# Kernel optimization log

Measured on AMD Instinct MI355X. Metric: run time of the kernel, lower is better.

Reference implementation:

```python
import jax, jax.numpy as jnp
import numpy as np

N, E, B, BLOCK = 100000, 1600000, 8, 12500
IN, HID, K, OUT = 128, 128, 4, 2
EPS = 1e-15


def setup_inputs() -> dict:
    key = jax.random.key(0)
    ks = jax.random.split(key, 14)
    x = jax.random.normal(ks[0], (N, IN), jnp.float32)
    # edges constrained within each graph's contiguous node block
    src = jax.random.randint(ks[1], (E,), 0, N)
    off = jax.random.randint(ks[2], (E,), 0, BLOCK)
    dst = (src // BLOCK) * BLOCK + off
    edge_index = jnp.stack([src, dst])
    batch = jnp.arange(N) // BLOCK
    s = 0.02
    params = dict(
        W_root1=jax.random.normal(ks[3], (IN, HID), jnp.float32) * s,
        W_rel1=jax.random.normal(ks[4], (IN, HID), jnp.float32) * s,
        b_rel1=jnp.zeros((HID,), jnp.float32),
        W_pool=jax.random.normal(ks[5], (HID, K), jnp.float32) * s,
        b_pool=jnp.zeros((K,), jnp.float32),
        W_rel3=jax.random.normal(ks[6], (HID, HID), jnp.float32) * s,
        b_rel3=jnp.zeros((HID,), jnp.float32),
        W_root3=jax.random.normal(ks[7], (HID, HID), jnp.float32) * s,
        W_lin1=jax.random.normal(ks[8], (HID, HID), jnp.float32) * s,
        b_lin1=jnp.zeros((HID,), jnp.float32),
        W_lin2=jax.random.normal(ks[9], (HID, OUT), jnp.float32) * s,
        b_lin2=jnp.zeros((OUT,), jnp.float32),
    )
    return dict(x=x, edge_index=edge_index, batch=batch, **params)


def _forward(x, edge_index, batch, W_root1, W_rel1, b_rel1, W_pool, b_pool,
             W_rel3, b_rel3, W_root3, W_lin1, b_lin1, W_lin2, b_lin2):
    src, dst = edge_index[0], edge_index[1]
    # GraphConv (aggr='add'): lin_rel(sum_j x_j) + lin_root(x)
    agg = jax.ops.segment_sum(x[src], dst, num_segments=N)  # [N, IN]
    h = jax.nn.relu(agg @ W_rel1 + b_rel1 + x @ W_root1)    # [N, HID]
    # cluster assignment
    s = jax.nn.softmax(h @ W_pool + b_pool, axis=-1)        # [N, K]
    # pooled node features: out[b] = S_b^T X_b  -> [B, K, HID]
    out = jax.ops.segment_sum(s[:, :, None] * h[:, None, :], batch, num_segments=B)
    # coarsened adjacency: out_adj[b] = S_b^T A_b S_b (A[dst, src] = 1 per edge)
    e_graph = batch[dst]
    contrib = s[dst][:, :, None] * s[src][:, None, :]       # [E, K, K]
    out_adj = jax.ops.segment_sum(contrib, e_graph, num_segments=B)  # [B, K, K]
    # mincut loss
    mincut_num = jnp.einsum('bkk->b', out_adj)
    deg = jax.ops.segment_sum(jnp.ones((E,), x.dtype), dst, num_segments=N)
    mincut_den = jax.ops.segment_sum(deg * jnp.sum(s * s, axis=-1), batch, num_segments=B)
    mc_loss = jnp.mean(-(mincut_num / mincut_den))
    # orthogonality loss
    ss = jax.ops.segment_sum(s[:, :, None] * s[:, None, :], batch, num_segments=B)  # [B,K,K]
    ss_norm = jnp.linalg.norm(ss, axis=(1, 2), keepdims=True)
    i_s = jnp.eye(K, dtype=x.dtype)
    o_loss = jnp.mean(jnp.linalg.norm(ss / ss_norm - i_s / jnp.sqrt(jnp.float32(K)), axis=(1, 2)))
    # fix and normalize coarsened adjacency
    out_adj = out_adj * (1.0 - i_s)  # zero diagonal
    d = jnp.sqrt(jnp.sum(out_adj, axis=-1)) + EPS  # [B, K]
    out_adj = out_adj / d[:, None, :] / d[:, :, None]
    # DenseGraphConv (aggr='add'): lin_rel(adj @ x) + lin_root(x)
    x2 = jnp.einsum('bkl,blc->bkc', out_adj, out) @ W_rel3 + b_rel3 + out @ W_root3
    x2 = jnp.mean(x2, axis=1)  # [B, HID]
    x2 = jax.nn.relu(x2 @ W_lin1 + b_lin1)
    logits = x2 @ W_lin2 + b_lin2
    return jax.nn.log_softmax(logits, axis=-1), mc_loss, o_loss, s, out_adj


def reference(x, edge_index, batch, W_root1, W_rel1, b_rel1, W_pool, b_pool,
              W_rel3, b_rel3, W_root3, W_lin1, b_lin1, W_lin2, b_lin2):
    return _forward(x, edge_index, batch, W_root1, W_rel1, b_rel1, W_pool, b_pool,
                    W_rel3, b_rel3, W_root3, W_lin1, b_lin1, W_lin2, b_lin2)
```

## Files before the change

### kernel.cpp

```cpp
#include <hip/hip_runtime.h>

#define NN     100000
#define EE     1600000
#define NB     8
#define BLK    12500
#define HID    128
#define KC     4
#define CHUNKS 196
#define NTILE  49
#define NBIN   392
#define GCAPS  5120

typedef __attribute__((ext_vector_type(8))) short bf16x8;
typedef __attribute__((ext_vector_type(4))) float f32x4;

__device__ __forceinline__ ushort f2bf(float f) {
  uint u = __float_as_uint(f);
  return (ushort)((u + 0x7FFFu + ((u >> 16) & 1u)) >> 16);
}
__device__ __forceinline__ float bf2f(ushort h) {
  return __uint_as_float(((uint)h) << 16);
}

#define GLL16(g, l) \
  __builtin_amdgcn_global_load_lds((const __attribute__((address_space(1))) void*)(g), \
                                   (__attribute__((address_space(3))) void*)(l), 16, 0, 0)

__global__ __launch_bounds__(256) void k_prep_x(const float4* __restrict__ x4,
                                                ushort* __restrict__ xb) {
  int i = blockIdx.x * 256 + threadIdx.x;
  float4 v = x4[i];
  ushort4 r;
  r.x = f2bf(v.x); r.y = f2bf(v.y); r.z = f2bf(v.z); r.w = f2bf(v.w);
  *(ushort4*)(xb + (size_t)i * 4) = r;
}

__global__ __launch_bounds__(256) void k_prep_w(const float* __restrict__ Wrel1,
                                                const float* __restrict__ Wroot1,
                                                ushort* __restrict__ Wt) {
  int col = blockIdx.x, k = threadIdx.x;
  float v = (k < 128) ? Wrel1[k * 128 + col] : Wroot1[(k - 128) * 128 + col];
  Wt[col * 256 + k] = f2bf(v);
}

__global__ __launch_bounds__(256) void k_bucket2(const int* __restrict__ ei,
                                                 int* __restrict__ sbcnt,
                                                 uint* __restrict__ gbuf) {
  __shared__ uint stage[8192];
  __shared__ int cnt[NBIN], start[NBIN + 1], rbase[NBIN];
  __shared__ int gtot[8], gb[8];
  const int t = threadIdx.x;
  for (int b = t; b < NBIN; b += 256) cnt[b] = 0;
  __syncthreads();
  const int e0 = blockIdx.x * 8192;
  uint pk[32]; int br[32];
#pragma unroll
  for (int i = 0; i < 32; ++i) {
    int e = e0 + i * 256 + t;
    bool val = (e < EE);
    int src = 0, dst = 0;
    if (val) {
      src = __builtin_nontemporal_load(ei + e);
      dst = __builtin_nontemporal_load(ei + EE + e);
    }
    int g = dst / BLK;
    int dl = dst - g * BLK;
    int sl = src - g * BLK;
    int bin = g * NTILE + (dl >> 8);
    pk[i] = ((uint)sl << 16) | (uint)dl;
    br[i] = val ? ((bin << 14) | atomicAdd(&cnt[bin], 1)) : -1;
  }
  __syncthreads();
  if (t < 8) {
    int s = 0;
    for (int k = 0; k < NTILE; ++k) s += cnt[t * NTILE + k];
    gtot[t] = s;
  }
  __syncthreads();
  if (t == 0) {
    int s = 0;
    for (int g = 0; g < 8; ++g) { gb[g] = s; s += gtot[g]; }
    start[NBIN] = s;
  }
  __syncthreads();
  if (t < 8) {
    int run = gb[t];
    for (int k = 0; k < NTILE; ++k) { start[t * NTILE + k] = run; run += cnt[t * NTILE + k]; }
  }
  __syncthreads();
  for (int b = t; b < NBIN; b += 256) rbase[b] = atomicAdd(&sbcnt[b], cnt[b]);
#pragma unroll
  for (int i = 0; i < 32; ++i) {
    if (br[i] >= 0) {
      int bin = br[i] >> 14, rank = br[i] & 16383;
      stage[start[bin] + rank] = pk[i];
    }
  }
  __syncthreads();
  for (int b = t; b < NBIN; b += 256) {
    const int n = cnt[b];
    const int s0 = start[b];
    uint* dst = gbuf + (size_t)b * GCAPS + rbase[b];
    for (int i = 0; i < n; ++i) dst[i] = stage[s0 + i];
  }
}

__global__ __launch_bounds__(512) void k_scan392(const int* __restrict__ sbcnt,
                                                 int* __restrict__ sbbase) {
  __shared__ int sd[512];
  const int t = threadIdx.x;
  int v = (t < NBIN) ? sbcnt[t] : 0;
  sd[t] = v;
  __syncthreads();
  for (int s = 1; s < 512; s <<= 1) {
    int x = (t >= s) ? sd[t - s] : 0;
    __syncthreads();
    sd[t] += x;
    __syncthreads();
  }
  if (t < NBIN) sbbase[t] = sd[t] - v;
}

__global__ __launch_bounds__(256) void k_csr_tile(const uint* __restrict__ gbuf,
                                                  const int* __restrict__ sbcnt,
                                                  const int* __restrict__ sbbase,
                                                  int* __restrict__ rowptr,
                                                  int* __restrict__ count,
                                                  int* __restrict__ csr) {
  const int g = blockIdx.x & 7;
  const int tile = blockIdx.x >> 3;
  const int bin = g * NTILE + tile;
  const int m = sbcnt[bin];
  const int base = sbbase[bin];
  const int n0t = tile * 256;
  const int nt = min(256, BLK - n0t);
  __shared__ uint ent[GCAPS];
  __shared__ ushort srt[GCAPS];
  __shared__ int cnt[256], scn[256], cur[256];
  const int t = threadIdx.x;
  cnt[t] = 0;
  __syncthreads();
  const uint* buf = gbuf + (size_t)bin * GCAPS;
  for (int i = t; i < m; i += 256) {
    uint pk = buf[i];
    ent[i] = pk;
    atomicAdd(&cnt[(int)(pk & 0xFFFFu) - n0t], 1);
  }
  __syncthreads();
  int v = cnt[t];
  scn[t] = v;
  __syncthreads();
  for (int s = 1; s < 256; s <<= 1) {
    int x = (t >= s) ? scn[t - s] : 0;
    __syncthreads();
    scn[t] += x;
    __syncthreads();
  }
  int excl = scn[t] - v;
  cur[t] = excl;
  if (t < nt) {
    rowptr[g * BLK + n0t + t] = base + excl;
    count[g * BLK + n0t + t] = v;
  }
  __syncthreads();
  for (int i = t; i < m; i += 256) {
    uint pk = ent[i];
    int p = atomicAdd(&cur[(int)(pk & 0xFFFFu) - n0t], 1);
    srt[p] = (ushort)(pk >> 16);
  }
  __syncthreads();
  const int nb = g * BLK;
  for (int i = t; i < m; i += 256)
    csr[base + i] = nb + (int)srt[i];
}

__global__ __launch_bounds__(256) void k_agg2(const ushort* __restrict__ xb,
                                              const int* __restrict__ count,
                                              const int* __restrict__ rowptr,
                                              const int* __restrict__ csr,
                                              const ushort* __restrict__ zrow,
                                              ushort* __restrict__ aggb) {
  const int xg = blockIdx.x & 7;
  const int j = blockIdx.x >> 3;
  const int half = threadIdx.x >> 5;
  const int lane = threadIdx.x & 31;
  const int ln = j * 8 + half;
  if (ln >= BLK) return;
  const int node = xg * BLK + ln;
  const int deg = count[node];
  const int* sl = csr + rowptr[node];
  int idx0 = (lane < deg) ? sl[lane] : 0;
  int idx1 = (32 + lane < deg) ? sl[32 + lane] : 0;
  const ushort* zr = zrow + lane * 4;

  float4 acc[8];
#pragma unroll
  for (int q = 0; q < 8; ++q) acc[q] = (float4){0.f, 0.f, 0.f, 0.f};

  const int nb8 = (deg + 7) >> 3;
  for (int b = 0; b < nb8; ++b) {
    const int e = b * 8;
    const ushort* ps[8];
#pragma unroll
    for (int q = 0; q < 8; ++q) {
      int ee = e + q;
      int si = (ee < 32) ? __shfl(idx0, ee, 32)
             : ((ee < 64) ? __shfl(idx1, ee - 32, 32)
                          : ((ee < deg) ? sl[ee] : 0));
      ps[q] = (ee < deg) ? (xb + (size_t)si * HID + lane * 4) : zr;
    }
    uint2 v[8];
#pragma unroll
    for (int q = 0; q < 8; ++q) v[q] = *(const uint2*)ps[q];
#pragma unroll
    for (int q = 0; q < 8; ++q) {
      acc[q].x += __uint_as_float(v[q].x << 16);
      acc[q].y += __uint_as_float(v[q].x & 0xFFFF0000u);
      acc[q].z += __uint_as_float(v[q].y << 16);
      acc[q].w += __uint_as_float(v[q].y & 0xFFFF0000u);
    }
  }

  float lo0 = 0.f, hi0 = 0.f, lo1 = 0.f, hi1 = 0.f;
#pragma unroll
  for (int q = 0; q < 8; ++q) { lo0 += acc[q].x; hi0 += acc[q].y; lo1 += acc[q].z; hi1 += acc[q].w; }
  ushort4 r;
  r.x = f2bf(lo0); r.y = f2bf(hi0); r.z = f2bf(lo1); r.w = f2bf(hi1);
  *(ushort4*)(aggb + (size_t)node * HID + lane * 4) = r;
}

__global__ __launch_bounds__(256) void k_gemm(
    const ushort* __restrict__ aggb, const ushort* __restrict__ xb,
    const ushort* __restrict__ Wt, const float* __restrict__ brel1,
    ushort* __restrict__ hbuf) {
  __shared__ ushort Aag_s[64][128];
  __shared__ ushort Ax_s[64][128];
  __shared__ ushort hLb[64][136];

  const int t = threadIdx.x;
  const int bi = blockIdx.x;
  const int bG = bi & 7;
  const int chunk = bi >> 3;
  const int node0 = bG * BLK + chunk * 64;
  int nrows = BLK - chunk * 64;
  if (nrows > 64) nrows = 64;

  const int w = t >> 6;
  const int l = t & 63;

  {
    const int sub = l >> 4;
    const int c16 = l & 15;
#pragma unroll
    for (int i = 0; i < 4; ++i) {
      const int j = w * 4 + i;
      const int row = j * 4 + sub;
      const int rs = (row < nrows) ? row : (nrows - 1);
      const int boff = (c16 * 16) ^ ((row & 7) << 4);
      const ushort* ga = aggb + (size_t)(node0 + rs) * HID + (boff >> 1);
      const ushort* gx = xb + (size_t)(node0 + rs) * HID + (boff >> 1);
      GLL16(ga, &Aag_s[j * 4][0]);
      GLL16(gx, &Ax_s[j * 4][0]);
    }
  }

  const int m16 = l & 15;
  const int gq = l >> 4;

  bf16x8 Breg[8][2];
#pragma unroll
  for (int kt = 0; kt < 8; ++kt)
#pragma unroll
    for (int fc = 0; fc < 2; ++fc)
      Breg[kt][fc] =
          *(const bf16x8*)(Wt + (size_t)(32 * w + 16 * fc + m16) * 256 + kt * 32 + 8 * gq);

  f32x4 acc[4][2];
#pragma unroll
  for (int fr = 0; fr < 4; ++fr)
#pragma unroll
    for (int fc = 0; fc < 2; ++fc) acc[fr][fc] = (f32x4){0.f, 0.f, 0.f, 0.f};

  asm volatile("s_waitcnt vmcnt(0)" ::: "memory");
  __syncthreads();

#pragma unroll
  for (int kt = 0; kt < 8; ++kt) {
    const int k4 = kt & 3;
    bf16x8 af[4];
#pragma unroll
    for (int fr = 0; fr < 4; ++fr) {
      const int r = 16 * fr + m16;
      const int ci = (k4 * 32 + gq * 8) ^ ((r & 7) << 3);
      af[fr] = (kt < 4) ? *(const bf16x8*)&Aag_s[r][ci]
                        : *(const bf16x8*)&Ax_s[r][ci];
    }
#pragma unroll
    for (int fr = 0; fr < 4; ++fr)
#pragma unroll
      for (int fc = 0; fc < 2; ++fc)
        acc[fr][fc] = __builtin_amdgcn_mfma_f32_16x16x32_bf16(af[fr], Breg[kt][fc],
                                                              acc[fr][fc], 0, 0, 0);
  }

  const float bc0 = brel1[32 * w + m16];
  const float bc1 = brel1[32 * w + 16 + m16];
#pragma unroll
  for (int fr = 0; fr < 4; ++fr)
#pragma unroll
    for (int fc = 0; fc < 2; ++fc)
#pragma unroll
      for (int r = 0; r < 4; ++r)
        hLb[16 * fr + 4 * gq + r][32 * w + 16 * fc + m16] =
            f2bf(fmaxf(acc[fr][fc][r] + (fc ? bc1 : bc0), 0.f));
  __syncthreads();

  {
    const int row = t >> 2;
    const int ch = (t & 3) * 32;
    if (row < nrows) {
      ushort* dst = hbuf + (size_t)(node0 + row) * HID + ch;
      const ushort* src = &hLb[row][ch];
#pragma unroll
      for (int q = 0; q < 4; ++q)
        *(bf16x8*)(dst + q * 8) = *(const bf16x8*)(src + q * 8);
    }
  }
}

__global__ __launch_bounds__(256) void k_epi(
    const ushort* __restrict__ hbuf, const float* __restrict__ Wpool,
    const float* __restrict__ bpool, const int* __restrict__ count,
    float* __restrict__ s_out, float* __restrict__ out_pool,
    float* __restrict__ ss_g, float* __restrict__ den_g) {
  __shared__ ushort hLb[64][136];
  __shared__ float outL[KC][HID];
  __shared__ float ssL[16];
  __shared__ float denL;

  const int t = threadIdx.x;
  const int bi = blockIdx.x;
  const int bG = bi & 7;
  const int chunk = bi >> 3;
  const int node0 = bG * BLK + chunk * 64;
  int nrows = BLK - chunk * 64;
  if (nrows > 64) nrows = 64;

  {
    const int row = t >> 2;
    const int ch = (t & 3) * 32;
    const int rs = (row < nrows) ? row : (nrows - 1);
    const ushort* src = hbuf + (size_t)(node0 + rs) * HID + ch;
    ushort* dst = &hLb[row][ch];
#pragma unroll
    for (int q = 0; q < 4; ++q)
      *(bf16x8*)(dst + q * 8) = *(const bf16x8*)(src + q * 8);
  }

  for (int i = t; i < KC * HID; i += 256) ((float*)outL)[i] = 0.f;
  if (t < 16) ssL[t] = 0.f;
  if (t == 0) denL = 0.f;
  __syncthreads();

  const int g4 = t >> 4;
  const int c0 = (t & 15) << 2;
  const int li = t & 15;

  float h[4][8];
#pragma unroll
  for (int r = 0; r < 4; ++r) {
    ushort4 v0 = *(const ushort4*)&hLb[g4 * 4 + r][c0];
    ushort4 v1 = *(const ushort4*)&hLb[g4 * 4 + r][c0 + 64];
    h[r][0] = bf2f(v0.x); h[r][1] = bf2f(v0.y); h[r][2] = bf2f(v0.z); h[r][3] = bf2f(v0.w);
    h[r][4] = bf2f(v1.x); h[r][5] = bf2f(v1.y); h[r][6] = bf2f(v1.z); h[r][7] = bf2f(v1.w);
  }

  float wp[8][4];
#pragma unroll
  for (int j = 0; j < 8; ++j) {
    int col = c0 + (j & 3) + (j >> 2) * 64;
    float4 v = *(const float4*)(Wpool + col * 4);
    wp[j][0] = v.x; wp[j][1] = v.y; wp[j][2] = v.z; wp[j][3] = v.w;
  }
  float pp[4][4];
#pragma unroll
  for (int r = 0; r < 4; ++r)
#pragma unroll
    for (int k = 0; k < 4; ++k) pp[r][k] = 0.f;
#pragma unroll
  for (int r = 0; r < 4; ++r)
#pragma unroll
    for (int j = 0; j < 8; ++j)
#pragma unroll
      for (int k = 0; k < 4; ++k) pp[r][k] = fmaf(h[r][j], wp[j][k], pp[r][k]);
#pragma unroll
  for (int m = 1; m <= 8; m <<= 1)
#pragma unroll
    for (int r = 0; r < 4; ++r)
#pragma unroll
      for (int k = 0; k < 4; ++k) pp[r][k] += __shfl_xor(pp[r][k], m);

  float4 bp4 = *(const float4*)bpool;
  float bp[4] = {bp4.x, bp4.y, bp4.z, bp4.w};
  float sv[4][4];
#pragma unroll
  for (int r = 0; r < 4; ++r) {
    float p[4];
#pragma unroll
    for (int k = 0; k < 4; ++k) p[k] = pp[r][k] + bp[k];
    float mx = fmaxf(fmaxf(p[0], p[1]), fmaxf(p[2], p[3]));
    float e0 = expf(p[0] - mx), e1 = expf(p[1] - mx), e2 = expf(p[2] - mx), e3 = expf(p[3] - mx);
    float inv = 1.f / (e0 + e1 + e2 + e3);
    float valid = (g4 * 4 + r < nrows) ? 1.f : 0.f;
    sv[r][0] = e0 * inv * valid; sv[r][1] = e1 * inv * valid;
    sv[r][2] = e2 * inv * valid; sv[r][3] = e3 * inv * valid;
  }

  {
    int rW = li >> 2, kW = li & 3;
    if (g4 * 4 + rW < nrows) {
      int node = node0 + g4 * 4 + rW;
      float val = 0.f;
#pragma unroll
      for (int rr = 0; rr < 4; ++rr)
#pragma unroll
        for (int kk = 0; kk < 4; ++kk)
          if (li == rr * 4 + kk) val = sv[rr][kk];
      s_out[node * 4 + kW] = val;
    }
  }

  {
    int k1 = li >> 2, k2 = li & 3;
    float a1[4], a2[4];
#pragma unroll
    for (int rr = 0; rr < 4; ++rr) {
      float v1 = 0.f, v2 = 0.f;
#pragma unroll
      for (int kk = 0; kk < 4; ++kk) {
        if (k1 == kk) v1 = sv[rr][kk];
        if (k2 == kk) v2 = sv[rr][kk];
      }
      a1[rr] = v1; a2[rr] = v2;
    }
    float ssv = a1[0] * a2[0] + a1[1] * a2[1] + a1[2] * a2[2] + a1[3] * a2[3];
    atomicAdd(&ssL[li], ssv);
  }

  if (li == 0) {
    float dent = 0.f;
#pragma unroll
    for (int rr = 0; rr < 4; ++rr) {
      int rowg = g4 * 4 + rr;
      if (rowg < nrows) {
        float dg = (float)count[node0 + rowg];
        dent += dg * (sv[rr][0] * sv[rr][0] + sv[rr][1] * sv[rr][1] +
                      sv[rr][2] * sv[rr][2] + sv[rr][3] * sv[rr][3]);
      }
    }
    atomicAdd(&denL, dent);
  }

  float po[4][8];
#pragma unroll
  for (int k = 0; k < 4; ++k)
#pragma unroll
    for (int c = 0; c < 8; ++c) po[k][c] = 0.f;
#pragma unroll
  for (int k = 0; k < 4; ++k)
#pragma unroll
    for (int rr = 0; rr < 4; ++rr)
#pragma unroll
      for (int c = 0; c < 8; ++c) po[k][c] = fmaf(sv[rr][k], h[rr][c], po[k][c]);
#pragma unroll
  for (int k = 0; k < 4; ++k)
#pragma unroll
    for (int c = 0; c < 8; ++c) {
      po[k][c] += __shfl_xor(po[k][c], 16);
      po[k][c] += __shfl_xor(po[k][c], 32);
    }
  if ((t & 63) < 16) {
#pragma unroll
    for (int k = 0; k < 4; ++k)
#pragma unroll
      for (int c = 0; c < 8; ++c)
        atomicAdd(&outL[k][c0 + (c & 3) + (c >> 2) * 64], po[k][c]);
  }

  __syncthreads();
  for (int i = t; i < KC * HID; i += 256)
    atomicAdd(&out_pool[bG * KC * HID + i], ((const float*)outL)[i]);
  if (t < 16) atomicAdd(&ss_g[bG * 16 + t], ssL[t]);
  if (t == 0) atomicAdd(&den_g[bG], denL);
}

__global__ __launch_bounds__(256) void k_adj2(const int* __restrict__ count,
                                              const int* __restrict__ rowptr,
                                              const int* __restrict__ csr,
                                              const float* __restrict__ s,
                                              const float* __restrict__ zf,
                                              float* __restrict__ adjraw) {
  __shared__ float accL[4][2][16];
  const int t = threadIdx.x;
  if (t < 128) ((float*)accL)[t] = 0.f;
  __syncthreads();
  const int node = blockIdx.x * 256 + t;
  const int g0 = (blockIdx.x * 256) / BLK;
  if (node < NN) {
    const int gi = node / BLK - g0;
    const int deg = count[node];
    const int* sl = csr + rowptr[node];
    float a[8][4];
#pragma unroll
    for (int q = 0; q < 8; ++q)
#pragma unroll
      for (int c = 0; c < 4; ++c) a[q][c] = 0.f;
    const int nb8 = (deg + 7) >> 3;
    for (int b = 0; b < nb8; ++b) {
      const float* p[8];
#pragma unroll
      for (int q = 0; q < 8; ++q) {
        int ee = b * 8 + q;
        int si = (ee < deg) ? sl[ee] : 0;
        p[q] = (ee < deg) ? (s + (size_t)si * 4) : zf;
      }
      float4 v[8];
#pragma unroll
      for (int q = 0; q < 8; ++q) v[q] = *(const float4*)p[q];
#pragma unroll
      for (int q = 0; q < 8; ++q) {
        a[q][0] += v[q].x; a[q][1] += v[q].y; a[q][2] += v[q].z; a[q][3] += v[q].w;
      }
    }
    float t0 = 0.f, t1 = 0.f, t2 = 0.f, t3 = 0.f;
#pragma unroll
    for (int q = 0; q < 8; ++q) { t0 += a[q][0]; t1 += a[q][1]; t2 += a[q][2]; t3 += a[q][3]; }
    float4 sn = *(const float4*)(s + (size_t)node * 4);
    float* base = accL[t >> 6][gi];
#pragma unroll
    for (int i = 0; i < 16; ++i) {
      int idx = (i + t) & 15;
      int hi = idx >> 2, lo = idx & 3;
      float a1 = (hi == 0) ? sn.x : (hi == 1) ? sn.y : (hi == 2) ? sn.z : sn.w;
      float b1 = (lo == 0) ? t0 : (lo == 1) ? t1 : (lo == 2) ? t2 : t3;
      atomicAdd(base + idx, a1 * b1);
    }
  }
  __syncthreads();
  if (t < 32) {
    int gi = t >> 4, i = t & 15, gg = g0 + gi;
    if (gg < NB) {
      float v = accL[0][gi][i] + accL[1][gi][i] + accL[2][gi][i] + accL[3][gi][i];
      atomicAdd(&adjraw[gg * 16 + i], v);
    }
  }
}

__global__ __launch_bounds__(128) void k_graph(
    const float* __restrict__ out_pool, const float* __restrict__ adjraw,
    const float* __restrict__ den_g, const float* __restrict__ ss_g,
    const float* __restrict__ Wrel3, const float* __restrict__ brel3,
    const float* __restrict__ Wroot3, const float* __restrict__ Wlin1,
    const float* __restrict__ blin1, const float* __restrict__ Wlin2,
    const float* __restrict__ blin2, float* __restrict__ d_out,
    float* __restrict__ scratch) {
  const int b = blockIdx.x, t = threadIdx.x;
  __shared__ float adjL[16], adjnL[16], dL[4];
  __shared__ float osL[128], msL[128], x2mL[128], x3L[128];
  if (t < 16) adjL[t] = adjraw[b * 16 + t];
  __syncthreads();
  if (t < 4) {
    float srow = 0.f;
#pragma unroll
    for (int l = 0; l < 4; ++l)
      if (l != t) srow += adjL[t * 4 + l];
    dL[t] = sqrtf(srow) + 1e-15f;
  }
  __syncthreads();
  if (t < 16) {
    int k1 = t >> 2, k2 = t & 3;
    float az = (k1 == k2) ? 0.f : adjL[t];
    float an = az / (dL[k2] * dL[k1]);
    adjnL[t] = an;
    d_out[400018 + b * 16 + t] = an;
  }
  __syncthreads();
  float o0 = out_pool[b * 512 + 0 * 128 + t];
  float o1 = out_pool[b * 512 + 1 * 128 + t];
  float o2 = out_pool[b * 512 + 2 * 128 + t];
  float o3 = out_pool[b * 512 + 3 * 128 + t];
  float m0 = adjnL[0] * o0 + adjnL[1] * o1 + adjnL[2] * o2 + adjnL[3] * o3;
  float m1 = adjnL[4] * o0 + adjnL[5] * o1 + adjnL[6] * o2 + adjnL[7] * o3;
  float m2 = adjnL[8] * o0 + adjnL[9] * o1 + adjnL[10] * o2 + adjnL[11] * o3;
  float m3 = adjnL[12] * o0 + adjnL[13] * o1 + adjnL[14] * o2 + adjnL[15] * o3;
  osL[t] = o0 + o1 + o2 + o3;
  msL[t] = m0 + m1 + m2 + m3;
  __syncthreads();
  float accc = brel3[t];
  for (int j = 0; j < 128; ++j)
    accc += 0.25f * (msL[j] * Wrel3[j * 128 + t] + osL[j] * Wroot3[j * 128 + t]);
  x2mL[t] = accc;
  __syncthreads();
  float a2 = blin1[t];
  for (int j = 0; j < 128; ++j) a2 += x2mL[j] * Wlin1[j * 128 + t];
  x3L[t] = fmaxf(a2, 0.f);
  __syncthreads();
  if (t < 2) {
    float lg = blin2[t];
    for (int j = 0; j < 128; ++j) lg += x3L[j] * Wlin2[j * 2 + t];
    scratch[b * 2 + t] = lg;
  }
  if (t == 0) {
    float tr = adjL[0] + adjL[5] + adjL[10] + adjL[15];
    scratch[16 + b] = tr / den_g[b];
    float n2 = 0.f;
    for (int i = 0; i < 16; ++i) { float v = ss_g[b * 16 + i]; n2 += v * v; }
    float nn = sqrtf(n2);
    float od = 0.f;
    for (int i = 0; i < 16; ++i) {
      float v = ss_g[b * 16 + i] / nn - (((i >> 2) == (i & 3)) ? 0.5f : 0.f);
      od += v * v;
    }
    scratch[24 + b] = sqrtf(od);
  }
}

__global__ void k_final(const float* __restrict__ scratch, float* __restrict__ d_out) {
  if (threadIdx.x == 0 && blockIdx.x == 0) {
    float mc = 0.f, oo = 0.f;
    for (int b = 0; b < NB; ++b) { mc += scratch[16 + b]; oo += scratch[24 + b]; }
    d_out[16] = -(mc / (float)NB);
    d_out[17] = oo / (float)NB;
    for (int b = 0; b < NB; ++b) {
      float l0 = scratch[2 * b], l1 = scratch[2 * b + 1];
      float m = fmaxf(l0, l1);
      float lse = m + logf(expf(l0 - m) + expf(l1 - m));
      d_out[2 * b] = l0 - lse;
      d_out[2 * b + 1] = l1 - lse;
    }
  }
}

extern "C" void kernel_launch(void* const* d_in, const int* in_sizes, int n_in,
                              void* d_out, int out_size, void* d_ws, size_t ws_size,
                              hipStream_t stream) {
  (void)in_sizes; (void)n_in; (void)out_size; (void)ws_size;
  const float* x      = (const float*)d_in[0];
  const int*   ei     = (const int*)d_in[1];
  const float* Wroot1 = (const float*)d_in[3];
  const float* Wrel1  = (const float*)d_in[4];
  const float* brel1  = (const float*)d_in[5];
  const float* Wpool  = (const float*)d_in[6];
  const float* bpool  = (const float*)d_in[7];
  const float* Wrel3  = (const float*)d_in[8];
  const float* brel3  = (const float*)d_in[9];
  const float* Wroot3 = (const float*)d_in[10];
  const float* Wlin1  = (const float*)d_in[11];
  const float* blin1  = (const float*)d_in[12];
  const float* Wlin2  = (const float*)d_in[13];
  const float* blin2  = (const float*)d_in[14];
  float* out = (float*)d_out;

  char* ws = (char*)d_ws;
  float*  out_pool = (float*)(ws + 0);
  float*  ss_g     = (float*)(ws + 16384);
  float*  adjraw   = (float*)(ws + 16896);
  float*  den_g    = (float*)(ws + 17408);
  float*  scratch  = (float*)(ws + 17440);
  int*    sbcnt    = (int*)(ws + 17568);
  ushort* zrow     = (ushort*)(ws + 19136);
  float*  zf       = (float*)(ws + 19392);
  int*    sbbase   = (int*)(ws + 19648);
  int*    count    = (int*)(ws + 21248);
  int*    rowptr   = (int*)(ws + 421248);
  ushort* Wt       = (ushort*)(ws + 821264);
  int*    csr      = (int*)(ws + 886800);
  ushort* xb       = (ushort*)(ws + 7286800);
  ushort* aggb     = (ushort*)(ws + 32886800);
  uint*   gbuf     = (uint*)(ws + 58486800);
  ushort* hbuf     = (ushort*)(ws + 66514960);

  hipMemsetAsync(ws, 0, 19648, stream);
  k_prep_x<<<12500, 256, 0, stream>>>((const float4*)x, xb);
  k_prep_w<<<128, 256, 0, stream>>>(Wrel1, Wroot1, Wt);
  k_bucket2<<<196, 256, 0, stream>>>(ei, sbcnt, gbuf);
  k_scan392<<<1, 512, 0, stream>>>(sbcnt, sbbase);
  k_csr_tile<<<NBIN, 256, 0, stream>>>(gbuf, sbcnt, sbbase, rowptr, count, csr);
  k_agg2<<<8 * ((BLK + 7) / 8), 256, 0, stream>>>(xb, count, rowptr, csr, zrow, aggb);
  k_gemm<<<NB * CHUNKS, 256, 0, stream>>>(aggb, xb, Wt, brel1, hbuf);
  k_epi<<<NB * CHUNKS, 256, 0, stream>>>(hbuf, Wpool, bpool, count, out + 18,
                                         out_pool, ss_g, den_g);
  k_adj2<<<(NN + 255) / 256, 256, 0, stream>>>(count, rowptr, csr, out + 18, zf, adjraw);
  k_graph<<<NB, 128, 0, stream>>>(out_pool, adjraw, den_g, ss_g, Wrel3, brel3, Wroot3,
                                  Wlin1, blin1, Wlin2, blin2, out, scratch);
  k_final<<<1, 64, 0, stream>>>(scratch, out);
}
```

Measured before the change: 206.6 us.

## Merge small kernels to cut launch count and drop memset

Folds the x and weight bf16 conversion plus the workspace zeroing into one prep kernel, which replaces the hipMemsetAsync. The separate 392-bin scan kernel is removed; each CSR tile block now computes its own base with a reduction over the preceding bin counts. The per-graph head kernel and the final reduction kernel are merged into a single 1024-thread block. This goes from eleven stream operations to seven, trading launch gaps for some redundant prefix-sum work in every CSR block and a single-block tail.

```diff
diff --git a/kernel.cpp b/kernel.cpp
--- a/kernel.cpp
+++ b/kernel.cpp
@@ -26,21 +26,27 @@
   __builtin_amdgcn_global_load_lds((const __attribute__((address_space(1))) void*)(g), \
                                    (__attribute__((address_space(3))) void*)(l), 16, 0, 0)
 
-__global__ __launch_bounds__(256) void k_prep_x(const float4* __restrict__ x4,
-                                                ushort* __restrict__ xb) {
-  int i = blockIdx.x * 256 + threadIdx.x;
-  float4 v = x4[i];
-  ushort4 r;
-  r.x = f2bf(v.x); r.y = f2bf(v.y); r.z = f2bf(v.z); r.w = f2bf(v.w);
-  *(ushort4*)(xb + (size_t)i * 4) = r;
-}
-
-__global__ __launch_bounds__(256) void k_prep_w(const float* __restrict__ Wrel1,
-                                                const float* __restrict__ Wroot1,
-                                                ushort* __restrict__ Wt) {
-  int col = blockIdx.x, k = threadIdx.x;
-  float v = (k < 128) ? Wrel1[k * 128 + col] : Wroot1[(k - 128) * 128 + col];
-  Wt[col * 256 + k] = f2bf(v);
+__global__ __launch_bounds__(256) void k_prep(const float4* __restrict__ x4,
+                                              ushort* __restrict__ xb,
+                                              const float* __restrict__ Wrel1,
+                                              const float* __restrict__ Wroot1,
+                                              ushort* __restrict__ Wt,
+                                              uint* __restrict__ zbase) {
+  const int bi = blockIdx.x;
+  const int t = threadIdx.x;
+  if (bi < 12500) {
+    int i = bi * 256 + t;
+    float4 v = x4[i];
+    ushort4 r;
+    r.x = f2bf(v.x); r.y = f2bf(v.y); r.z = f2bf(v.z); r.w = f2bf(v.w);
+    *(ushort4*)(xb + (size_t)i * 4) = r;
+  } else if (bi < 12628) {
+    int col = bi - 12500, k = t;
+    float v = (k < 128) ? Wrel1[k * 128 + col] : Wroot1[(k - 128) * 128 + col];
+    Wt[col * 256 + k] = f2bf(v);
+  } else {
+    for (int i = t; i < 4912; i += 256) zbase[i] = 0u;
+  }
 }
 
 __global__ __launch_bounds__(256) void k_bucket2(const int* __restrict__ ei,
@@ -105,25 +111,8 @@
   }
 }
 
-__global__ __launch_bounds__(512) void k_scan392(const int* __restrict__ sbcnt,
-                                                 int* __restrict__ sbbase) {
-  __shared__ int sd[512];
-  const int t = threadIdx.x;
-  int v = (t < NBIN) ? sbcnt[t] : 0;
-  sd[t] = v;
-  __syncthreads();
-  for (int s = 1; s < 512; s <<= 1) {
-    int x = (t >= s) ? sd[t - s] : 0;
-    __syncthreads();
-    sd[t] += x;
-    __syncthreads();
-  }
-  if (t < NBIN) sbbase[t] = sd[t] - v;
-}
-
 __global__ __launch_bounds__(256) void k_csr_tile(const uint* __restrict__ gbuf,
                                                   const int* __restrict__ sbcnt,
-                                                  const int* __restrict__ sbbase,
                                                   int* __restrict__ rowptr,
                                                   int* __restrict__ count,
                                                   int* __restrict__ csr) {
@@ -131,13 +120,24 @@
   const int tile = blockIdx.x >> 3;
   const int bin = g * NTILE + tile;
   const int m = sbcnt[bin];
-  const int base = sbbase[bin];
   const int n0t = tile * 256;
   const int nt = min(256, BLK - n0t);
   __shared__ uint ent[GCAPS];
   __shared__ ushort srt[GCAPS];
   __shared__ int cnt[256], scn[256], cur[256];
+  __shared__ int red[256];
   const int t = threadIdx.x;
+  {
+    int partial = 0;
+    for (int i = t; i < bin; i += 256) partial += sbcnt[i];
+    red[t] = partial;
+    __syncthreads();
+    for (int off = 128; off > 0; off >>= 1) {
+      if (t < off) red[t] += red[t + off];
+      __syncthreads();
+    }
+  }
+  const int base = red[0];
   cnt[t] = 0;
   __syncthreads();
   const uint* buf = gbuf + (size_t)bin * GCAPS;
@@ -556,7 +556,7 @@
   }
 }
 
-__global__ __launch_bounds__(128) void k_graph(
+__global__ __launch_bounds__(1024) void k_tail(
     const float* __restrict__ out_pool, const float* __restrict__ adjraw,
     const float* __restrict__ den_g, const float* __restrict__ ss_g,
     const float* __restrict__ Wrel3, const float* __restrict__ brel3,
@@ -564,69 +564,68 @@
     const float* __restrict__ blin1, const float* __restrict__ Wlin2,
     const float* __restrict__ blin2, float* __restrict__ d_out,
     float* __restrict__ scratch) {
-  const int b = blockIdx.x, t = threadIdx.x;
-  __shared__ float adjL[16], adjnL[16], dL[4];
-  __shared__ float osL[128], msL[128], x2mL[128], x3L[128];
-  if (t < 16) adjL[t] = adjraw[b * 16 + t];
-  __syncthreads();
-  if (t < 4) {
+  const int g = threadIdx.x >> 7;
+  const int tt = threadIdx.x & 127;
+  __shared__ float adjL[NB][16], adjnL[NB][16], dL[NB][4];
+  __shared__ float osL[NB][128], msL[NB][128], x2mL[NB][128], x3L[NB][128];
+  if (tt < 16) adjL[g][tt] = adjraw[g * 16 + tt];
+  __syncthreads();
+  if (tt < 4) {
     float srow = 0.f;
 #pragma unroll
     for (int l = 0; l < 4; ++l)
-      if (l != t) srow += adjL[t * 4 + l];
-    dL[t] = sqrtf(srow) + 1e-15f;
-  }
-  __syncthreads();
-  if (t < 16) {
-    int k1 = t >> 2, k2 = t & 3;
-    float az = (k1 == k2) ? 0.f : adjL[t];
-    float an = az / (dL[k2] * dL[k1]);
-    adjnL[t] = an;
-    d_out[400018 + b * 16 + t] = an;
-  }
-  __syncthreads();
-  float o0 = out_pool[b * 512 + 0 * 128 + t];
-  float o1 = out_pool[b * 512 + 1 * 128 + t];
-  float o2 = out_pool[b * 512 + 2 * 128 + t];
-  float o3 = out_pool[b * 512 + 3 * 128 + t];
-  float m0 = adjnL[0] * o0 + adjnL[1] * o1 + adjnL[2] * o2 + adjnL[3] * o3;
-  float m1 = adjnL[4] * o0 + adjnL[5] * o1 + adjnL[6] * o2 + adjnL[7] * o3;
-  float m2 = adjnL[8] * o0 + adjnL[9] * o1 + adjnL[10] * o2 + adjnL[11] * o3;
-  float m3 = adjnL[12] * o0 + adjnL[13] * o1 + adjnL[14] * o2 + adjnL[15] * o3;
-  osL[t] = o0 + o1 + o2 + o3;
-  msL[t] = m0 + m1 + m2 + m3;
-  __syncthreads();
-  float accc = brel3[t];
+      if (l != tt) srow += adjL[g][tt * 4 + l];
+    dL[g][tt] = sqrtf(srow) + 1e-15f;
+  }
+  __syncthreads();
+  if (tt < 16) {
+    int k1 = tt >> 2, k2 = tt & 3;
+    float az = (k1 == k2) ? 0.f : adjL[g][tt];
+    float an = az / (dL[g][k2] * dL[g][k1]);
+    adjnL[g][tt] = an;
+    d_out[400018 + g * 16 + tt] = an;
+  }
+  __syncthreads();
+  float o0 = out_pool[g * 512 + 0 * 128 + tt];
+  float o1 = out_pool[g * 512 + 1 * 128 + tt];
+  float o2 = out_pool[g * 512 + 2 * 128 + tt];
+  float o3 = out_pool[g * 512 + 3 * 128 + tt];
+  float m0 = adjnL[g][0] * o0 + adjnL[g][1] * o1 + adjnL[g][2] * o2 + adjnL[g][3] * o3;
+  float m1 = adjnL[g][4] * o0 + adjnL[g][5] * o1 + adjnL[g][6] * o2 + adjnL[g][7] * o3;
+  float m2 = adjnL[g][8] * o0 + adjnL[g][9] * o1 + adjnL[g][10] * o2 + adjnL[g][11] * o3;
+  float m3 = adjnL[g][12] * o0 + adjnL[g][13] * o1 + adjnL[g][14] * o2 + adjnL[g][15] * o3;
+  osL[g][tt] = o0 + o1 + o2 + o3;
+  msL[g][tt] = m0 + m1 + m2 + m3;
+  __syncthreads();
+  float accc = brel3[tt];
   for (int j = 0; j < 128; ++j)
-    accc += 0.25f * (msL[j] * Wrel3[j * 128 + t] + osL[j] * Wroot3[j * 128 + t]);
-  x2mL[t] = accc;
-  __syncthreads();
-  float a2 = blin1[t];
-  for (int j = 0; j < 128; ++j) a2 += x2mL[j] * Wlin1[j * 128 + t];
-  x3L[t] = fmaxf(a2, 0.f);
-  __syncthreads();
-  if (t < 2) {
-    float lg = blin2[t];
-    for (int j = 0; j < 128; ++j) lg += x3L[j] * Wlin2[j * 2 + t];
-    scratch[b * 2 + t] = lg;
-  }
-  if (t == 0) {
-    float tr = adjL[0] + adjL[5] + adjL[10] + adjL[15];
-    scratch[16 + b] = tr / den_g[b];
+    accc += 0.25f * (msL[g][j] * Wrel3[j * 128 + tt] + osL[g][j] * Wroot3[j * 128 + tt]);
+  x2mL[g][tt] = accc;
+  __syncthreads();
+  float a2 = blin1[tt];
+  for (int j = 0; j < 128; ++j) a2 += x2mL[g][j] * Wlin1[j * 128 + tt];
+  x3L[g][tt] = fmaxf(a2, 0.f);
+  __syncthreads();
+  if (tt < 2) {
+    float lg = blin2[tt];
+    for (int j = 0; j < 128; ++j) lg += x3L[g][j] * Wlin2[j * 2 + tt];
+    scratch[g * 2 + tt] = lg;
+  }
+  if (tt == 0) {
+    float tr = adjL[g][0] + adjL[g][5] + adjL[g][10] + adjL[g][15];
+    scratch[16 + g] = tr / den_g[g];
     float n2 = 0.f;
-    for (int i = 0; i < 16; ++i) { float v = ss_g[b * 16 + i]; n2 += v * v; }
+    for (int i = 0; i < 16; ++i) { float v = ss_g[g * 16 + i]; n2 += v * v; }
     float nn = sqrtf(n2);
     float od = 0.f;
     for (int i = 0; i < 16; ++i) {
-      float v = ss_g[b * 16 + i] / nn - (((i >> 2) == (i & 3)) ? 0.5f : 0.f);
+      float v = ss_g[g * 16 + i] / nn - (((i >> 2) == (i & 3)) ? 0.5f : 0.f);
       od += v * v;
     }
-    scratch[24 + b] = sqrtf(od);
-  }
-}
-
-__global__ void k_final(const float* __restrict__ scratch, float* __restrict__ d_out) {
-  if (threadIdx.x == 0 && blockIdx.x == 0) {
+    scratch[24 + g] = sqrtf(od);
+  }
+  __syncthreads();
+  if (threadIdx.x == 0) {
     float mc = 0.f, oo = 0.f;
     for (int b = 0; b < NB; ++b) { mc += scratch[16 + b]; oo += scratch[24 + b]; }
     d_out[16] = -(mc / (float)NB);
@@ -670,7 +669,6 @@
   int*    sbcnt    = (int*)(ws + 17568);
   ushort* zrow     = (ushort*)(ws + 19136);
   float*  zf       = (float*)(ws + 19392);
-  int*    sbbase   = (int*)(ws + 19648);
   int*    count    = (int*)(ws + 21248);
   int*    rowptr   = (int*)(ws + 421248);
   ushort* Wt       = (ushort*)(ws + 821264);
@@ -680,18 +678,15 @@
   uint*   gbuf     = (uint*)(ws + 58486800);
   ushort* hbuf     = (ushort*)(ws + 66514960);
 
-  hipMemsetAsync(ws, 0, 19648, stream);
-  k_prep_x<<<12500, 256, 0, stream>>>((const float4*)x, xb);
-  k_prep_w<<<128, 256, 0, stream>>>(Wrel1, Wroot1, Wt);
+  k_prep<<<12629, 256, 0, stream>>>((const float4*)x, xb, Wrel1, Wroot1, Wt,
+                                    (uint*)ws);
   k_bucket2<<<196, 256, 0, stream>>>(ei, sbcnt, gbuf);
-  k_scan392<<<1, 512, 0, stream>>>(sbcnt, sbbase);
-  k_csr_tile<<<NBIN, 256, 0, stream>>>(gbuf, sbcnt, sbbase, rowptr, count, csr);
+  k_csr_tile<<<NBIN, 256, 0, stream>>>(gbuf, sbcnt, rowptr, count, csr);
   k_agg2<<<8 * ((BLK + 7) / 8), 256, 0, stream>>>(xb, count, rowptr, csr, zrow, aggb);
   k_gemm<<<NB * CHUNKS, 256, 0, stream>>>(aggb, xb, Wt, brel1, hbuf);
   k_epi<<<NB * CHUNKS, 256, 0, stream>>>(hbuf, Wpool, bpool, count, out + 18,
                                          out_pool, ss_g, den_g);
   k_adj2<<<(NN + 255) / 256, 256, 0, stream>>>(count, rowptr, csr, out + 18, zf, adjraw);
-  k_graph<<<NB, 128, 0, stream>>>(out_pool, adjraw, den_g, ss_g, Wrel3, brel3, Wroot3,
-                                  Wlin1, blin1, Wlin2, blin2, out, scratch);
-  k_final<<<1, 64, 0, stream>>>(scratch, out);
-}
+  k_tail<<<1, 1024, 0, stream>>>(out_pool, adjraw, den_g, ss_g, Wrel3, brel3, Wroot3,
+                                 Wlin1, blin1, Wlin2, blin2, out, scratch);
+}
```

Result: no change. 202.6 us (-1.9%).
